# Kernel tuning notes

Measured on AMD Instinct MI355X. Metric: run time of the kernel, lower is better.

Reference implementation:

```python
import jax, jax.numpy as jnp
import numpy as np

B, T, F, H, S = 4096, 200, 76, 128, 17


def setup_inputs() -> dict:
    key = jax.random.key(0)
    ks = jax.random.split(key, 10)
    kf = 1.0 / np.sqrt(H)
    return {
        "x": jax.random.normal(ks[0], (B, T, F), dtype=jnp.float32),
        "static": jax.random.normal(ks[1], (B, S), dtype=jnp.float32),
        "h0": jax.random.normal(ks[2], (B, H), dtype=jnp.float32),
        "c0": jax.random.normal(ks[3], (B, H), dtype=jnp.float32),
        "W_ih": jax.random.uniform(ks[4], (4 * H, F), jnp.float32, -kf, kf),
        "W_hh": jax.random.uniform(ks[5], (4 * H, H), jnp.float32, -kf, kf),
        "b_ih": jax.random.uniform(ks[6], (4 * H,), jnp.float32, -kf, kf),
        "b_hh": jax.random.uniform(ks[7], (4 * H,), jnp.float32, -kf, kf),
        "W_lin": jax.random.uniform(ks[8], (1, H + S), jnp.float32, -kf, kf),
        "b_lin": jax.random.uniform(ks[9], (1,), jnp.float32, -kf, kf),
    }


def reference(x, static, h0, c0, W_ih, W_hh, b_ih, b_hh, W_lin, b_lin):
    # Precompute input projections for all timesteps in one big GEMM: [B,T,4H]
    x_proj = jnp.einsum("btf,gf->btg", x, W_ih) + b_ih
    xs = jnp.swapaxes(x_proj, 0, 1)  # time-major [T, B, 4H]

    def step(carry, xp):
        h, c = carry
        gates = xp + h @ W_hh.T + b_hh  # [B, 4H]
        i, f, g, o = jnp.split(gates, 4, axis=-1)
        i, f, o = jax.nn.sigmoid(i), jax.nn.sigmoid(f), jax.nn.sigmoid(o)
        c = f * c + i * jnp.tanh(g)
        h = o * jnp.tanh(c)
        return (h, c), None

    (h, c), _ = jax.lax.scan(step, (h0, c0), xs)
    full = jnp.concatenate([h, static], axis=1)  # [B, H+S]
    predictions = full @ W_lin.T + b_lin  # [B, 1]
    return predictions
```

## Files before the change

### kernel.cpp

```cpp
#include <hip/hip_runtime.h>
#include <hip/hip_bf16.h>

#define B_TOT   4096
#define T_LEN   200
#define F_IN    76
#define H_DIM   128
#define S_DIM   17
#define BLK_B   16
#define NTHREADS 512
#define NT_CHUNK 8
#define NCHUNK  (T_LEN / NT_CHUNK)
#define XPITCH  104
#define HPITCH  136
#define ROW_F4  ((NT_CHUNK * F_IN) / 4)
#define TOT_F4  (BLK_B * ROW_F4)
#define PF_N    5

static_assert(NCHUNK * NT_CHUNK == T_LEN, "chunking must cover T exactly");

using f32x4 = __attribute__((ext_vector_type(4))) float;
using s16x8 = __attribute__((ext_vector_type(8))) short;
using s16x4 = __attribute__((ext_vector_type(4))) short;

#if __has_builtin(__builtin_amdgcn_exp2f)
#define EXP2(v) __builtin_amdgcn_exp2f(v)
#else
#define EXP2(v) exp2f(v)
#endif
#if __has_builtin(__builtin_amdgcn_rcpf)
#define RCP(v) __builtin_amdgcn_rcpf(v)
#else
#define RCP(v) (1.0f / (v))
#endif

__device__ __forceinline__ short f2bf(float f) {
    union { float f; unsigned u; } v; v.f = f;
    unsigned r = v.u + 0x7FFFu + ((v.u >> 16) & 1u);
    return (short)(r >> 16);
}
__device__ __forceinline__ float bf2f(short s) {
    union { unsigned u; float f; } v;
    v.u = ((unsigned)(unsigned short)s) << 16;
    return v.f;
}

__global__ __launch_bounds__(NTHREADS, 2) void lstm_fused(
    const float* __restrict__ x,    const float* __restrict__ stat,
    const float* __restrict__ h0,   const float* __restrict__ c0,
    const float* __restrict__ W_ih, const float* __restrict__ W_hh,
    const float* __restrict__ b_ih, const float* __restrict__ b_hh,
    const float* __restrict__ W_lin, const float* __restrict__ b_lin,
    float* __restrict__ out)
{
    __shared__ __align__(16) short xbuf[2][NT_CHUNK][BLK_B][XPITCH];
    __shared__ __align__(16) short hbuf[2][BLK_B][HPITCH];

    const int tid  = threadIdx.x;
    const int lane = tid & 63;
    const int wave = tid >> 6;
    const int lrow = lane & 15;
    const int lk8  = (lane >> 4) << 3;
    const int r0   = (lane >> 4) << 2;
    const int b0   = blockIdx.x * BLK_B;
    const int hb   = wave << 4;

    const float C1 = 1.44269504088896f;
    const float gs[4] = { -C1, -C1, -2.0f * C1, -C1 };

    s16x8 wih[4][3], whh[4][4];
    float bias[4];
#pragma unroll
    for (int nt = 0; nt < 4; ++nt) {
        const int col = nt * H_DIM + hb + lrow;
        const float s = gs[nt];
#pragma unroll
        for (int kt = 0; kt < 3; ++kt) {
            s16x8 f;
#pragma unroll
            for (int j = 0; j < 8; ++j) {
                int k = kt * 32 + lk8 + j;
                float v = (k < F_IN) ? W_ih[col * F_IN + k] * s : 0.0f;
                f[j] = f2bf(v);
            }
            wih[nt][kt] = f;
        }
#pragma unroll
        for (int kt = 0; kt < 4; ++kt) {
            s16x8 f;
#pragma unroll
            for (int j = 0; j < 8; ++j) {
                int k = kt * 32 + lk8 + j;
                f[j] = f2bf(W_hh[col * H_DIM + k] * s);
            }
            whh[nt][kt] = f;
        }
        bias[nt] = (b_ih[col] + b_hh[col]) * s;
    }

    float c[4];
#pragma unroll
    for (int r = 0; r < 4; ++r)
        c[r] = c0[(b0 + r0 + r) * H_DIM + hb + lrow];

    for (int i = tid; i < BLK_B * H_DIM; i += NTHREADS) {
        int row = i >> 7, cc = i & 127;
        hbuf[0][row][cc] = f2bf(h0[(b0 + row) * H_DIM + cc]);
    }
    for (int i = tid; i < 2 * NT_CHUNK * BLK_B * (96 - F_IN); i += NTHREADS) {
        int rem = i;
        int f  = rem % (96 - F_IN); rem /= (96 - F_IN);
        int row = rem % BLK_B;      rem /= BLK_B;
        int tt = rem % NT_CHUNK;    rem /= NT_CHUNK;
        xbuf[rem][tt][row][F_IN + f] = 0;
    }

    f32x4 pf[PF_N];
    auto issue = [&](int ch) {
#pragma unroll
        for (int i = 0; i < PF_N; ++i) {
            int idx = tid + i * NTHREADS;
            if (idx < TOT_F4) {
                int row = idx / ROW_F4;
                int s4  = idx - row * ROW_F4;
                pf[i] = *(const f32x4*)(x + (size_t)(b0 + row) * (T_LEN * F_IN)
                                          + (size_t)ch * (NT_CHUNK * F_IN) + s4 * 4);
            }
        }
    };
    auto commit = [&](int buf) {
#pragma unroll
        for (int i = 0; i < PF_N; ++i) {
            int idx = tid + i * NTHREADS;
            if (idx < TOT_F4) {
                int row = idx / ROW_F4;
                int q   = (idx - row * ROW_F4) * 4;
                int tp  = q / F_IN;
                int f0  = q - tp * F_IN;
                s16x4 v = { f2bf(pf[i].x), f2bf(pf[i].y), f2bf(pf[i].z), f2bf(pf[i].w) };
                *(s16x4*)&xbuf[buf][tp][row][f0] = v;
            }
        }
    };

    issue(0);
    commit(0);
    __syncthreads();

    int cur = 0, xcur = 0;
    for (int ch = 0; ch < NCHUNK; ++ch) {
        if (ch + 1 < NCHUNK) issue(ch + 1);
        for (int tt = 0; tt < NT_CHUNK; ++tt) {
            s16x8 ax[3], ah[4];
#pragma unroll
            for (int kt = 0; kt < 3; ++kt)
                ax[kt] = *(const s16x8*)&xbuf[xcur][tt][lrow][kt * 32 + lk8];
#pragma unroll
            for (int kt = 0; kt < 4; ++kt)
                ah[kt] = *(const s16x8*)&hbuf[cur][lrow][kt * 32 + lk8];

            f32x4 acc[4];
#pragma unroll
            for (int nt = 0; nt < 4; ++nt)
                acc[nt] = (f32x4){ bias[nt], bias[nt], bias[nt], bias[nt] };
#pragma unroll
            for (int nt = 0; nt < 4; ++nt) {
#pragma unroll
                for (int kt = 0; kt < 3; ++kt)
                    acc[nt] = __builtin_amdgcn_mfma_f32_16x16x32_bf16(ax[kt], wih[nt][kt], acc[nt], 0, 0, 0);
#pragma unroll
                for (int kt = 0; kt < 4; ++kt)
                    acc[nt] = __builtin_amdgcn_mfma_f32_16x16x32_bf16(ah[kt], whh[nt][kt], acc[nt], 0, 0, 0);
            }

            float hv[4];
#pragma unroll
            for (int r = 0; r < 4; ++r) {
                float A  = EXP2(fminf(acc[0][r], 24.f));
                float Bv = EXP2(fminf(acc[1][r], 24.f));
                float E  = EXP2(fminf(acc[2][r], 24.f));
                float Dv = EXP2(fminf(acc[3][r], 24.f));
                float p1 = 1.f + A, p2 = 1.f + Bv, p3 = 1.f + E;
                float q13 = p1 * p3;
                float num = c[r] * q13 + (2.f - p3) * p2;
                float cn  = num * RCP(q13 * p2);
                c[r] = cn;
                float Ec = EXP2(fminf(cn * (-2.f * C1), 24.f));
                float u  = 1.f + Ec;
                hv[r] = (2.f - u) * RCP((1.f + Dv) * u);
            }

            if (tt == NT_CHUNK - 1 && ch + 1 < NCHUNK) commit(xcur ^ 1);

#pragma unroll
            for (int r = 0; r < 4; ++r)
                hbuf[cur ^ 1][r0 + r][hb + lrow] = f2bf(hv[r]);
            __syncthreads();
            cur ^= 1;
        }
        xcur ^= 1;
    }

    if (tid < BLK_B) {
        const int row = tid;
        float a = b_lin[0];
        for (int k = 0; k < H_DIM; ++k)
            a += bf2f(hbuf[cur][row][k]) * W_lin[k];
        for (int s = 0; s < S_DIM; ++s)
            a += stat[(b0 + row) * S_DIM + s] * W_lin[H_DIM + s];
        out[b0 + row] = a;
    }
}

extern "C" void kernel_launch(void* const* d_in, const int* in_sizes, int n_in,
                              void* d_out, int out_size, void* d_ws, size_t ws_size,
                              hipStream_t stream) {
    const float* xx   = (const float*)d_in[0];
    const float* st   = (const float*)d_in[1];
    const float* h0   = (const float*)d_in[2];
    const float* c0   = (const float*)d_in[3];
    const float* Wih  = (const float*)d_in[4];
    const float* Whh  = (const float*)d_in[5];
    const float* bih  = (const float*)d_in[6];
    const float* bhh  = (const float*)d_in[7];
    const float* Wlin = (const float*)d_in[8];
    const float* blin = (const float*)d_in[9];
    float* o = (float*)d_out;

    lstm_fused<<<B_TOT / BLK_B, NTHREADS, 0, stream>>>(
        xx, st, h0, c0, Wih, Whh, bih, bhh, Wlin, blin, o);
}
```

Baseline: 233.0 us.

## Software-pipeline input projection off the recurrent critical path in LSTM kernel

Computes the x·W_ih MFMA contribution for the next timestep while the gate nonlinearities of the current step run. This takes three of the seven MFMAs per gate tile off the serial h-dependency chain. It also moves the prefetch issue later in the chunk, uses hardware packed bf16 conversion, and precomputes the LDS offsets for the prefetch scatter. The step loop is unrolled by two so the h buffer indices are constant, and the exp clamps on the gate inputs are removed, which changes overflow handling. The cost is more live registers for the prefetched projections under a 2-blocks-per-SM launch bound.

```diff
diff --git a/kernel.cpp b/kernel.cpp
--- a/kernel.cpp
+++ b/kernel.cpp
@@ -10,17 +10,15 @@
 #define NTHREADS 512
 #define NT_CHUNK 8
 #define NCHUNK  (T_LEN / NT_CHUNK)
-#define XPITCH  104
+#define XPITCH  96
 #define HPITCH  136
 #define ROW_F4  ((NT_CHUNK * F_IN) / 4)
-#define TOT_F4  (BLK_B * ROW_F4)
 #define PF_N    5
 
 static_assert(NCHUNK * NT_CHUNK == T_LEN, "chunking must cover T exactly");
 
 using f32x4 = __attribute__((ext_vector_type(4))) float;
 using s16x8 = __attribute__((ext_vector_type(8))) short;
-using s16x4 = __attribute__((ext_vector_type(4))) short;
 
 #if __has_builtin(__builtin_amdgcn_exp2f)
 #define EXP2(v) __builtin_amdgcn_exp2f(v)
@@ -43,6 +41,11 @@
     v.u = ((unsigned)(unsigned short)s) << 16;
     return v.f;
 }
+__device__ __forceinline__ unsigned cvt_pk_bf16(float lo, float hi) {
+    unsigned r;
+    asm("v_cvt_pk_bf16_f32 %0, %1, %2" : "=v"(r) : "v"(lo), "v"(hi));
+    return r;
+}
 
 __global__ __launch_bounds__(NTHREADS, 2) void lstm_fused(
     const float* __restrict__ x,    const float* __restrict__ stat,
@@ -106,105 +109,135 @@
         int row = i >> 7, cc = i & 127;
         hbuf[0][row][cc] = f2bf(h0[(b0 + row) * H_DIM + cc]);
     }
-    for (int i = tid; i < 2 * NT_CHUNK * BLK_B * (96 - F_IN); i += NTHREADS) {
+    for (int i = tid; i < 2 * NT_CHUNK * BLK_B * (XPITCH - F_IN); i += NTHREADS) {
         int rem = i;
-        int f  = rem % (96 - F_IN); rem /= (96 - F_IN);
-        int row = rem % BLK_B;      rem /= BLK_B;
-        int tt = rem % NT_CHUNK;    rem /= NT_CHUNK;
+        int f   = rem % (XPITCH - F_IN); rem /= (XPITCH - F_IN);
+        int row = rem % BLK_B;           rem /= BLK_B;
+        int tt  = rem % NT_CHUNK;        rem /= NT_CHUNK;
         xbuf[rem][tt][row][F_IN + f] = 0;
+    }
+
+    const int prow = tid >> 5;
+    const int pidx = tid & 31;
+    const float* psrc = x + (size_t)(b0 + prow) * (T_LEN * F_IN) + pidx * 4;
+    int ldsoff[PF_N];
+#pragma unroll
+    for (int i = 0; i < PF_N; ++i) {
+        int s4 = pidx + 32 * i;
+        int q  = 4 * s4;
+        int tp = (q * 863) >> 16;
+        int f0 = q - 76 * tp;
+        ldsoff[i] = (tp * BLK_B + prow) * XPITCH + f0;
     }
 
     f32x4 pf[PF_N];
     auto issue = [&](int ch) {
-#pragma unroll
-        for (int i = 0; i < PF_N; ++i) {
-            int idx = tid + i * NTHREADS;
-            if (idx < TOT_F4) {
-                int row = idx / ROW_F4;
-                int s4  = idx - row * ROW_F4;
-                pf[i] = *(const f32x4*)(x + (size_t)(b0 + row) * (T_LEN * F_IN)
-                                          + (size_t)ch * (NT_CHUNK * F_IN) + s4 * 4);
+        const float* p = psrc + (size_t)ch * (NT_CHUNK * F_IN);
+#pragma unroll
+        for (int i = 0; i < PF_N; ++i)
+            if (i < PF_N - 1 || pidx < ROW_F4 - 4 * 32)
+                pf[i] = *(const f32x4*)(p + i * 128);
+    };
+    auto commit = [&](int buf) {
+        short* xb0 = &xbuf[buf][0][0][0];
+#pragma unroll
+        for (int i = 0; i < PF_N; ++i)
+            if (i < PF_N - 1 || pidx < ROW_F4 - 4 * 32) {
+                unsigned lo = cvt_pk_bf16(pf[i].x, pf[i].y);
+                unsigned hi = cvt_pk_bf16(pf[i].z, pf[i].w);
+                unsigned long long v = ((unsigned long long)hi << 32) | lo;
+                *(unsigned long long*)(xb0 + ldsoff[i]) = v;
             }
-        }
-    };
-    auto commit = [&](int buf) {
-#pragma unroll
-        for (int i = 0; i < PF_N; ++i) {
-            int idx = tid + i * NTHREADS;
-            if (idx < TOT_F4) {
-                int row = idx / ROW_F4;
-                int q   = (idx - row * ROW_F4) * 4;
-                int tp  = q / F_IN;
-                int f0  = q - tp * F_IN;
-                s16x4 v = { f2bf(pf[i].x), f2bf(pf[i].y), f2bf(pf[i].z), f2bf(pf[i].w) };
-                *(s16x4*)&xbuf[buf][tp][row][f0] = v;
-            }
-        }
     };
 
     issue(0);
     commit(0);
     __syncthreads();
 
-    int cur = 0, xcur = 0;
+    s16x8 axr[3];
+    f32x4 xa[4];
+    auto load_ax = [&](int buf, int tt) {
+#pragma unroll
+        for (int kt = 0; kt < 3; ++kt)
+            axr[kt] = *(const s16x8*)&xbuf[buf][tt][lrow][kt * 32 + lk8];
+    };
+    auto calc_xa = [&]() {
+#pragma unroll
+        for (int nt = 0; nt < 4; ++nt) {
+            f32x4 t = (f32x4){ bias[nt], bias[nt], bias[nt], bias[nt] };
+#pragma unroll
+            for (int kt = 0; kt < 3; ++kt)
+                t = __builtin_amdgcn_mfma_f32_16x16x32_bf16(axr[kt], wih[nt][kt], t, 0, 0, 0);
+            xa[nt] = t;
+        }
+    };
+
+    load_ax(0, 0);
+    calc_xa();
+
+#define STEP(CUR, TT)                                                          \
+    {                                                                          \
+        s16x8 ah[4];                                                           \
+        _Pragma("unroll")                                                      \
+        for (int kt = 0; kt < 4; ++kt)                                         \
+            ah[kt] = *(const s16x8*)&hbuf[CUR][lrow][kt * 32 + lk8];           \
+        f32x4 acc[4];                                                          \
+        _Pragma("unroll")                                                      \
+        for (int nt = 0; nt < 4; ++nt) {                                       \
+            f32x4 t = xa[nt];                                                  \
+            _Pragma("unroll")                                                  \
+            for (int kt = 0; kt < 4; ++kt)                                     \
+                t = __builtin_amdgcn_mfma_f32_16x16x32_bf16(ah[kt], whh[nt][kt], t, 0, 0, 0); \
+            acc[nt] = t;                                                       \
+        }                                                                      \
+        if ((TT) < NT_CHUNK - 1) { load_ax(xc, (TT) + 1); calc_xa(); }         \
+        float hv[4];                                                           \
+        _Pragma("unroll")                                                      \
+        for (int r = 0; r < 4; ++r) {                                          \
+            float A  = EXP2(acc[0][r]);                                        \
+            float Bv = EXP2(acc[1][r]);                                        \
+            float E  = EXP2(acc[2][r]);                                        \
+            float Dv = EXP2(acc[3][r]);                                        \
+            float sE = 1.f - E, p3 = 1.f + E;                                  \
+            float p1 = 1.f + A, p2 = 1.f + Bv;                                 \
+            float q13 = p1 * p3;                                               \
+            float num = fmaf(c[r], q13, sE * p2);                              \
+            float cn  = num * RCP(q13 * p2);                                   \
+            c[r] = cn;                                                         \
+            float ea = fminf(cn * (-2.f * C1), 80.f);                          \
+            float Ec = EXP2(ea);                                               \
+            float sEc = 1.f - Ec, uEc = 1.f + Ec;                              \
+            hv[r] = sEc * RCP((1.f + Dv) * uEc);                               \
+        }                                                                      \
+        if ((TT) == 0 && ch + 1 < NCHUNK) issue(ch + 1);                       \
+        if ((TT) == NT_CHUNK - 1 && ch + 1 < NCHUNK) commit(xc ^ 1);           \
+        unsigned q01 = cvt_pk_bf16(hv[0], hv[1]);                              \
+        unsigned q23 = cvt_pk_bf16(hv[2], hv[3]);                              \
+        unsigned short* hp = (unsigned short*)&hbuf[(CUR) ^ 1][r0][hb + lrow]; \
+        hp[0 * HPITCH] = (unsigned short)q01;                                  \
+        hp[1 * HPITCH] = (unsigned short)(q01 >> 16);                          \
+        hp[2 * HPITCH] = (unsigned short)q23;                                  \
+        hp[3 * HPITCH] = (unsigned short)(q23 >> 16);                          \
+        __syncthreads();                                                       \
+        if ((TT) == NT_CHUNK - 1 && ch + 1 < NCHUNK) {                         \
+            load_ax(xc ^ 1, 0); calc_xa();                                     \
+        }                                                                      \
+    }
+
     for (int ch = 0; ch < NCHUNK; ++ch) {
-        if (ch + 1 < NCHUNK) issue(ch + 1);
-        for (int tt = 0; tt < NT_CHUNK; ++tt) {
-            s16x8 ax[3], ah[4];
-#pragma unroll
-            for (int kt = 0; kt < 3; ++kt)
-                ax[kt] = *(const s16x8*)&xbuf[xcur][tt][lrow][kt * 32 + lk8];
-#pragma unroll
-            for (int kt = 0; kt < 4; ++kt)
-                ah[kt] = *(const s16x8*)&hbuf[cur][lrow][kt * 32 + lk8];
-
-            f32x4 acc[4];
-#pragma unroll
-            for (int nt = 0; nt < 4; ++nt)
-                acc[nt] = (f32x4){ bias[nt], bias[nt], bias[nt], bias[nt] };
-#pragma unroll
-            for (int nt = 0; nt < 4; ++nt) {
-#pragma unroll
-                for (int kt = 0; kt < 3; ++kt)
-                    acc[nt] = __builtin_amdgcn_mfma_f32_16x16x32_bf16(ax[kt], wih[nt][kt], acc[nt], 0, 0, 0);
-#pragma unroll
-                for (int kt = 0; kt < 4; ++kt)
-                    acc[nt] = __builtin_amdgcn_mfma_f32_16x16x32_bf16(ah[kt], whh[nt][kt], acc[nt], 0, 0, 0);
-            }
-
-            float hv[4];
-#pragma unroll
-            for (int r = 0; r < 4; ++r) {
-                float A  = EXP2(fminf(acc[0][r], 24.f));
-                float Bv = EXP2(fminf(acc[1][r], 24.f));
-                float E  = EXP2(fminf(acc[2][r], 24.f));
-                float Dv = EXP2(fminf(acc[3][r], 24.f));
-                float p1 = 1.f + A, p2 = 1.f + Bv, p3 = 1.f + E;
-                float q13 = p1 * p3;
-                float num = c[r] * q13 + (2.f - p3) * p2;
-                float cn  = num * RCP(q13 * p2);
-                c[r] = cn;
-                float Ec = EXP2(fminf(cn * (-2.f * C1), 24.f));
-                float u  = 1.f + Ec;
-                hv[r] = (2.f - u) * RCP((1.f + Dv) * u);
-            }
-
-            if (tt == NT_CHUNK - 1 && ch + 1 < NCHUNK) commit(xcur ^ 1);
-
-#pragma unroll
-            for (int r = 0; r < 4; ++r)
-                hbuf[cur ^ 1][r0 + r][hb + lrow] = f2bf(hv[r]);
-            __syncthreads();
-            cur ^= 1;
-        }
-        xcur ^= 1;
-    }
+        const int xc = ch & 1;
+        for (int tt = 0; tt < NT_CHUNK; tt += 2) {
+            STEP(0, tt)
+            STEP(1, tt + 1)
+        }
+    }
+#undef STEP
 
     if (tid < BLK_B) {
         const int row = tid;
         float a = b_lin[0];
         for (int k = 0; k < H_DIM; ++k)
-            a += bf2f(hbuf[cur][row][k]) * W_lin[k];
+            a += bf2f(hbuf[0][row][k]) * W_lin[k];
         for (int s = 0; s < S_DIM; ++s)
             a += stat[(b0 + row) * S_DIM + s] * W_lin[H_DIM + s];
         out[b0 + row] = a;
```

Measured after the change: 207.9 us. 10.8% less time.

## Specialize waves: half compute x-projection ahead, half run nonlinearity and state

Applied to the files above, without the earlier changes.

Splits the 8 waves into two roles. Waves 4-7 precompute the next step's input projection (with the bias folded into W_ih as an extra hi/lo bf16 column) and the recurrent GEMM for the upper hidden half. Waves 0-3 own the cell state for both halves, apply the nonlinearities, write h, and handle the global prefetch of x. The goal is to take the input GEMM and bias off the serial recurrence path. In exchange, each step now needs two barriers and passes gates through LDS. The chunk size drops to 4, the h buffer becomes single-buffered, and the bf16 conversion now uses a packed cvt instruction.

```diff
diff --git a/kernel.cpp b/kernel.cpp
--- a/kernel.cpp
+++ b/kernel.cpp
@@ -8,19 +8,17 @@
 #define S_DIM   17
 #define BLK_B   16
 #define NTHREADS 512
-#define NT_CHUNK 8
+#define NT_CHUNK 4
 #define NCHUNK  (T_LEN / NT_CHUNK)
 #define XPITCH  104
 #define HPITCH  136
-#define ROW_F4  ((NT_CHUNK * F_IN) / 4)
-#define TOT_F4  (BLK_B * ROW_F4)
+#define XHALF   (NT_CHUNK * BLK_B * XPITCH)
 #define PF_N    5
 
 static_assert(NCHUNK * NT_CHUNK == T_LEN, "chunking must cover T exactly");
 
 using f32x4 = __attribute__((ext_vector_type(4))) float;
 using s16x8 = __attribute__((ext_vector_type(8))) short;
-using s16x4 = __attribute__((ext_vector_type(4))) short;
 
 #if __has_builtin(__builtin_amdgcn_exp2f)
 #define EXP2(v) __builtin_amdgcn_exp2f(v)
@@ -43,6 +41,32 @@
     v.u = ((unsigned)(unsigned short)s) << 16;
     return v.f;
 }
+__device__ __forceinline__ unsigned cvt_pk_bf16(float lo, float hi) {
+    unsigned r;
+    asm("v_cvt_pk_bf16_f32 %0, %1, %2" : "=v"(r) : "v"(lo), "v"(hi));
+    return r;
+}
+__device__ __forceinline__ f32x4 mfma16x32(s16x8 a, s16x8 b, f32x4 c) {
+    return __builtin_amdgcn_mfma_f32_16x16x32_bf16(a, b, c, 0, 0, 0);
+}
+
+#define LDS_BARRIER() asm volatile("s_waitcnt lgkmcnt(0)\n\ts_barrier" ::: "memory")
+
+#define NONLIN4(G0, G1, G2, G3, CR, HV)                                 \
+    _Pragma("unroll")                                                   \
+    for (int r = 0; r < 4; ++r) {                                       \
+        float A  = EXP2((G0)[r]);                                       \
+        float Bv = EXP2((G1)[r]);                                       \
+        float E  = EXP2((G2)[r]);                                       \
+        float Dv = EXP2((G3)[r]);                                       \
+        float p1 = 1.f + A, p2 = 1.f + Bv, p3 = 1.f + E;                \
+        float q13 = p1 * p3;                                            \
+        float num = fmaf((CR)[r], q13, (1.f - E) * p2);                 \
+        float cn  = num * RCP(q13 * p2);                                \
+        (CR)[r] = cn;                                                   \
+        float Ec = EXP2(fminf(cn * (-2.f * C1), 80.f));                 \
+        (HV)[r] = (1.f - Ec) * RCP((1.f + Dv) * (1.f + Ec));            \
+    }
 
 __global__ __launch_bounds__(NTHREADS, 2) void lstm_fused(
     const float* __restrict__ x,    const float* __restrict__ stat,
@@ -52,159 +76,230 @@
     const float* __restrict__ W_lin, const float* __restrict__ b_lin,
     float* __restrict__ out)
 {
-    __shared__ __align__(16) short xbuf[2][NT_CHUNK][BLK_B][XPITCH];
-    __shared__ __align__(16) short hbuf[2][BLK_B][HPITCH];
+    __shared__ __align__(16) short xbuf[2 * XHALF];
+    __shared__ __align__(16) short hbuf[BLK_B * HPITCH];
+    __shared__ __align__(16) f32x4 gbuf[4 * 4 * 64];
+    __shared__ __align__(16) f32x4 xabuf[4 * 4 * 64];
+    __shared__ __align__(16) s16x8 wihbuf[4 * 4 * 2 * 3 * 64];
 
     const int tid  = threadIdx.x;
     const int lane = tid & 63;
-    const int wave = tid >> 6;
+    const int w    = tid >> 6;
+    const int p    = w & 3;
+    const bool isB = w >= 4;
     const int lrow = lane & 15;
     const int lk8  = (lane >> 4) << 3;
     const int r0   = (lane >> 4) << 2;
     const int b0   = blockIdx.x * BLK_B;
-    const int hb   = wave << 4;
+    const int hbA  = p * 16;
+    const int hbB  = 64 + p * 16;
+    const int hbOwn = isB ? hbB : hbA;
 
     const float C1 = 1.44269504088896f;
     const float gs[4] = { -C1, -C1, -2.0f * C1, -C1 };
 
-    s16x8 wih[4][3], whh[4][4];
-    float bias[4];
+    s16x8 whh[4][4];
 #pragma unroll
     for (int nt = 0; nt < 4; ++nt) {
-        const int col = nt * H_DIM + hb + lrow;
+        const int col = nt * H_DIM + hbOwn + lrow;
         const float s = gs[nt];
-#pragma unroll
-        for (int kt = 0; kt < 3; ++kt) {
-            s16x8 f;
-#pragma unroll
-            for (int j = 0; j < 8; ++j) {
-                int k = kt * 32 + lk8 + j;
-                float v = (k < F_IN) ? W_ih[col * F_IN + k] * s : 0.0f;
-                f[j] = f2bf(v);
-            }
-            wih[nt][kt] = f;
-        }
 #pragma unroll
         for (int kt = 0; kt < 4; ++kt) {
             s16x8 f;
 #pragma unroll
-            for (int j = 0; j < 8; ++j) {
-                int k = kt * 32 + lk8 + j;
-                f[j] = f2bf(W_hh[col * H_DIM + k] * s);
+            for (int j = 0; j < 8; ++j)
+                f[j] = f2bf(W_hh[col * H_DIM + kt * 32 + lk8 + j] * s);
+            whh[nt][kt] = f;
+        }
+    }
+
+    if (isB) {
+#pragma unroll
+        for (int nt = 0; nt < 4; ++nt) {
+#pragma unroll
+            for (int cg = 0; cg < 2; ++cg) {
+                const int col = nt * H_DIM + (cg ? hbB : hbA) + lrow;
+                const float s = gs[nt];
+                const float bsc = (b_ih[col] + b_hh[col]) * s;
+                const short bhi = f2bf(bsc);
+                const short blo = f2bf(bsc - bf2f(bhi));
+#pragma unroll
+                for (int kt = 0; kt < 3; ++kt) {
+                    s16x8 f;
+#pragma unroll
+                    for (int j = 0; j < 8; ++j) {
+                        const int k = kt * 32 + lk8 + j;
+                        short v;
+                        if (k < F_IN)     v = f2bf(W_ih[col * F_IN + k] * s);
+                        else if (k == 76) v = bhi;
+                        else if (k == 77) v = blo;
+                        else              v = 0;
+                        f[j] = v;
+                    }
+                    wihbuf[(((p * 4 + nt) * 2 + cg) * 3 + kt) * 64 + lane] = f;
+                }
             }
-            whh[nt][kt] = f;
-        }
-        bias[nt] = (b_ih[col] + b_hh[col]) * s;
-    }
-
-    float c[4];
-#pragma unroll
-    for (int r = 0; r < 4; ++r)
-        c[r] = c0[(b0 + r0 + r) * H_DIM + hb + lrow];
-
-    for (int i = tid; i < BLK_B * H_DIM; i += NTHREADS) {
-        int row = i >> 7, cc = i & 127;
-        hbuf[0][row][cc] = f2bf(h0[(b0 + row) * H_DIM + cc]);
-    }
-    for (int i = tid; i < 2 * NT_CHUNK * BLK_B * (96 - F_IN); i += NTHREADS) {
-        int rem = i;
-        int f  = rem % (96 - F_IN); rem /= (96 - F_IN);
-        int row = rem % BLK_B;      rem /= BLK_B;
-        int tt = rem % NT_CHUNK;    rem /= NT_CHUNK;
-        xbuf[rem][tt][row][F_IN + f] = 0;
+        }
+    }
+
+    float c0r[4], c1r[4];
+    int ldsoff[PF_N];
+    const float* psrc = x;
+    const int pidx_m = tid & 15;
+    if (!isB) {
+#pragma unroll
+        for (int r = 0; r < 4; ++r) {
+            c0r[r] = c0[(b0 + r0 + r) * H_DIM + hbA + lrow];
+            c1r[r] = c0[(b0 + r0 + r) * H_DIM + hbB + lrow];
+        }
+        for (int i = tid; i < BLK_B * H_DIM; i += 256) {
+            int row = i >> 7, cc = i & 127;
+            hbuf[row * HPITCH + cc] = f2bf(h0[(b0 + row) * H_DIM + cc]);
+        }
+        for (int i = tid; i < 2 * NT_CHUNK * BLK_B * (XPITCH - F_IN); i += 256) {
+            int f  = i % (XPITCH - F_IN);
+            int rs = i / (XPITCH - F_IN);
+            xbuf[rs * XPITCH + F_IN + f] = (f < 2) ? (short)0x3F80 : (short)0;
+        }
+        const int prow = tid >> 4;
+        psrc = x + (size_t)(b0 + prow) * (T_LEN * F_IN) + pidx_m * 4;
+#pragma unroll
+        for (int i = 0; i < PF_N; ++i) {
+            int s4 = pidx_m + 16 * i, q = 4 * s4;
+            int tp = (q * 863) >> 16;
+            int f0 = q - 76 * tp;
+            ldsoff[i] = (tp * BLK_B + prow) * XPITCH + f0;
+        }
     }
 
     f32x4 pf[PF_N];
     auto issue = [&](int ch) {
-#pragma unroll
-        for (int i = 0; i < PF_N; ++i) {
-            int idx = tid + i * NTHREADS;
-            if (idx < TOT_F4) {
-                int row = idx / ROW_F4;
-                int s4  = idx - row * ROW_F4;
-                pf[i] = *(const f32x4*)(x + (size_t)(b0 + row) * (T_LEN * F_IN)
-                                          + (size_t)ch * (NT_CHUNK * F_IN) + s4 * 4);
+        const float* pp = psrc + (size_t)ch * (NT_CHUNK * F_IN);
+#pragma unroll
+        for (int i = 0; i < PF_N; ++i)
+            if (i < PF_N - 1 || pidx_m < 12)
+                pf[i] = *(const f32x4*)(pp + i * 64);
+    };
+    auto commit = [&](int half) {
+        short* xb0 = xbuf + half * XHALF;
+#pragma unroll
+        for (int i = 0; i < PF_N; ++i)
+            if (i < PF_N - 1 || pidx_m < 12) {
+                unsigned lo = cvt_pk_bf16(pf[i].x, pf[i].y);
+                unsigned hi = cvt_pk_bf16(pf[i].z, pf[i].w);
+                unsigned long long v = ((unsigned long long)hi << 32) | lo;
+                *(unsigned long long*)(xb0 + ldsoff[i]) = v;
             }
-        }
     };
-    auto commit = [&](int buf) {
-#pragma unroll
-        for (int i = 0; i < PF_N; ++i) {
-            int idx = tid + i * NTHREADS;
-            if (idx < TOT_F4) {
-                int row = idx / ROW_F4;
-                int q   = (idx - row * ROW_F4) * 4;
-                int tp  = q / F_IN;
-                int f0  = q - tp * F_IN;
-                s16x4 v = { f2bf(pf[i].x), f2bf(pf[i].y), f2bf(pf[i].z), f2bf(pf[i].w) };
-                *(s16x4*)&xbuf[buf][tp][row][f0] = v;
+
+    if (!isB) { issue(0); commit(0); }
+    __syncthreads();
+
+    s16x8 axr[3];
+    f32x4 xaB[4];
+    auto load_axr = [&](int half, int slot) {
+#pragma unroll
+        for (int kt = 0; kt < 3; ++kt)
+            axr[kt] = *(const s16x8*)&xbuf[half * XHALF
+                        + (slot * BLK_B + lrow) * XPITCH + kt * 32 + lk8];
+    };
+    auto do_xproj = [&]() {
+        const f32x4 z = { 0.f, 0.f, 0.f, 0.f };
+#pragma unroll
+        for (int nt = 0; nt < 4; ++nt) {
+            const int base = ((p * 4 + nt) * 2 + 0) * 3;
+            f32x4 t = mfma16x32(axr[0], wihbuf[(base + 0) * 64 + lane], z);
+            t = mfma16x32(axr[1], wihbuf[(base + 1) * 64 + lane], t);
+            t = mfma16x32(axr[2], wihbuf[(base + 2) * 64 + lane], t);
+            xabuf[(p * 4 + nt) * 64 + lane] = t;
+        }
+#pragma unroll
+        for (int nt = 0; nt < 4; ++nt) {
+            const int base = ((p * 4 + nt) * 2 + 1) * 3;
+            f32x4 t = mfma16x32(axr[0], wihbuf[(base + 0) * 64 + lane], z);
+            t = mfma16x32(axr[1], wihbuf[(base + 1) * 64 + lane], t);
+            t = mfma16x32(axr[2], wihbuf[(base + 2) * 64 + lane], t);
+            xaB[nt] = t;
+        }
+    };
+
+    if (isB) { load_axr(0, 0); do_xproj(); }
+    LDS_BARRIER();
+
+#pragma unroll 1
+    for (int ch = 0; ch < NCHUNK; ++ch) {
+        const int xc = ch & 1;
+#pragma unroll 1
+        for (int tt = 0; tt < NT_CHUNK; ++tt) {
+            s16x8 ah[4];
+#pragma unroll
+            for (int kt = 0; kt < 4; ++kt)
+                ah[kt] = *(const s16x8*)&hbuf[lrow * HPITCH + kt * 32 + lk8];
+            f32x4 acc[4];
+            if (!isB) {
+#pragma unroll
+                for (int nt = 0; nt < 4; ++nt) {
+                    f32x4 t = xabuf[(p * 4 + nt) * 64 + lane];
+                    t = mfma16x32(ah[0], whh[nt][0], t);
+                    t = mfma16x32(ah[1], whh[nt][1], t);
+                    t = mfma16x32(ah[2], whh[nt][2], t);
+                    t = mfma16x32(ah[3], whh[nt][3], t);
+                    acc[nt] = t;
+                }
+            } else {
+#pragma unroll
+                for (int nt = 0; nt < 4; ++nt) {
+                    f32x4 t = xaB[nt];
+                    t = mfma16x32(ah[0], whh[nt][0], t);
+                    t = mfma16x32(ah[1], whh[nt][1], t);
+                    t = mfma16x32(ah[2], whh[nt][2], t);
+                    t = mfma16x32(ah[3], whh[nt][3], t);
+                    acc[nt] = t;
+                }
+#pragma unroll
+                for (int nt = 0; nt < 4; ++nt)
+                    gbuf[(p * 4 + nt) * 64 + lane] = acc[nt];
+                const int ttn = (tt + 1) & (NT_CHUNK - 1);
+                const int xcn = (tt == NT_CHUNK - 1) ? (xc ^ 1) : xc;
+                load_axr(xcn, ttn);
             }
-        }
-    };
-
-    issue(0);
-    commit(0);
-    __syncthreads();
-
-    int cur = 0, xcur = 0;
-    for (int ch = 0; ch < NCHUNK; ++ch) {
-        if (ch + 1 < NCHUNK) issue(ch + 1);
-        for (int tt = 0; tt < NT_CHUNK; ++tt) {
-            s16x8 ax[3], ah[4];
-#pragma unroll
-            for (int kt = 0; kt < 3; ++kt)
-                ax[kt] = *(const s16x8*)&xbuf[xcur][tt][lrow][kt * 32 + lk8];
-#pragma unroll
-            for (int kt = 0; kt < 4; ++kt)
-                ah[kt] = *(const s16x8*)&hbuf[cur][lrow][kt * 32 + lk8];
-
-            f32x4 acc[4];
-#pragma unroll
-            for (int nt = 0; nt < 4; ++nt)
-                acc[nt] = (f32x4){ bias[nt], bias[nt], bias[nt], bias[nt] };
-#pragma unroll
-            for (int nt = 0; nt < 4; ++nt) {
-#pragma unroll
-                for (int kt = 0; kt < 3; ++kt)
-                    acc[nt] = __builtin_amdgcn_mfma_f32_16x16x32_bf16(ax[kt], wih[nt][kt], acc[nt], 0, 0, 0);
-#pragma unroll
-                for (int kt = 0; kt < 4; ++kt)
-                    acc[nt] = __builtin_amdgcn_mfma_f32_16x16x32_bf16(ah[kt], whh[nt][kt], acc[nt], 0, 0, 0);
+            LDS_BARRIER();
+            if (!isB) {
+                if (tt == 0 && ch + 1 < NCHUNK) issue(ch + 1);
+                f32x4 gB[4];
+#pragma unroll
+                for (int nt = 0; nt < 4; ++nt)
+                    gB[nt] = gbuf[(p * 4 + nt) * 64 + lane];
+                float hv0[4], hv1[4];
+                NONLIN4(acc[0], acc[1], acc[2], acc[3], c0r, hv0);
+                NONLIN4(gB[0],  gB[1],  gB[2],  gB[3],  c1r, hv1);
+                unsigned u01 = cvt_pk_bf16(hv0[0], hv0[1]);
+                unsigned u23 = cvt_pk_bf16(hv0[2], hv0[3]);
+                unsigned v01 = cvt_pk_bf16(hv1[0], hv1[1]);
+                unsigned v23 = cvt_pk_bf16(hv1[2], hv1[3]);
+                unsigned short* hp0 = (unsigned short*)&hbuf[r0 * HPITCH + hbA + lrow];
+                hp0[0 * HPITCH] = (unsigned short)u01;
+                hp0[1 * HPITCH] = (unsigned short)(u01 >> 16);
+                hp0[2 * HPITCH] = (unsigned short)u23;
+                hp0[3 * HPITCH] = (unsigned short)(u23 >> 16);
+                unsigned short* hp1 = (unsigned short*)&hbuf[r0 * HPITCH + hbB + lrow];
+                hp1[0 * HPITCH] = (unsigned short)v01;
+                hp1[1 * HPITCH] = (unsigned short)(v01 >> 16);
+                hp1[2 * HPITCH] = (unsigned short)v23;
+                hp1[3 * HPITCH] = (unsigned short)(v23 >> 16);
+                if (tt == 2 && ch + 1 < NCHUNK) commit(xc ^ 1);
+            } else {
+                if (ch * NT_CHUNK + tt < T_LEN - 1) do_xproj();
             }
-
-            float hv[4];
-#pragma unroll
-            for (int r = 0; r < 4; ++r) {
-                float A  = EXP2(fminf(acc[0][r], 24.f));
-                float Bv = EXP2(fminf(acc[1][r], 24.f));
-                float E  = EXP2(fminf(acc[2][r], 24.f));
-                float Dv = EXP2(fminf(acc[3][r], 24.f));
-                float p1 = 1.f + A, p2 = 1.f + Bv, p3 = 1.f + E;
-                float q13 = p1 * p3;
-                float num = c[r] * q13 + (2.f - p3) * p2;
-                float cn  = num * RCP(q13 * p2);
-                c[r] = cn;
-                float Ec = EXP2(fminf(cn * (-2.f * C1), 24.f));
-                float u  = 1.f + Ec;
-                hv[r] = (2.f - u) * RCP((1.f + Dv) * u);
-            }
-
-            if (tt == NT_CHUNK - 1 && ch + 1 < NCHUNK) commit(xcur ^ 1);
-
-#pragma unroll
-            for (int r = 0; r < 4; ++r)
-                hbuf[cur ^ 1][r0 + r][hb + lrow] = f2bf(hv[r]);
-            __syncthreads();
-            cur ^= 1;
-        }
-        xcur ^= 1;
+            LDS_BARRIER();
+        }
     }
 
     if (tid < BLK_B) {
         const int row = tid;
         float a = b_lin[0];
         for (int k = 0; k < H_DIM; ++k)
-            a += bf2f(hbuf[cur][row][k]) * W_lin[k];
+            a += bf2f(hbuf[row * HPITCH + k]) * W_lin[k];
         for (int s = 0; s < S_DIM; ++s)
             a += stat[(b0 + row) * S_DIM + s] * W_lin[H_DIM + s];
         out[b0 + row] = a;
```

Measured after the change: 278.8 us. +19.6%, slower.
